# Kernel tuning notes

Hardware: AMD Instinct MI355X
Metric: run time of the kernel (lower is better)

## Reference

```python
import jax, jax.numpy as jnp
import numpy as np

EPS = 1e-12  # matches torch.nn.functional.normalize default eps

def _l2_normalize(x):
    # F.normalize: x / max(||x||_2, eps)
    n = jnp.linalg.norm(x, axis=-1, keepdims=True)
    return x / jnp.maximum(n, EPS)

def setup_inputs() -> dict:
    key = jax.random.key(0)
    k_z, k_e = jax.random.split(key)
    B, N, D, K = 8, 4096, 64, 8192
    z = jax.random.normal(k_z, (B, N, D), dtype=jnp.float32)
    # nn.Embedding weight initialized uniform(-1/K, 1/K)
    embedding = jax.random.uniform(k_e, (K, D), dtype=jnp.float32,
                                   minval=-1.0 / K, maxval=1.0 / K)
    return {"z": z, "embedding": embedding, "temperature": 1.0}

def reference(z, embedding, temperature):
    z_norm = _l2_normalize(z)                      # (B,N,D)
    codebook = _l2_normalize(embedding)            # (K,D)
    sim = jnp.einsum('bnd,kd->bnk', z_norm, codebook)  # (B,N,K)
    dists = 1.0 - sim
    probs = jax.nn.softmax(-dists / temperature, axis=-1)  # (B,N,K)
    z_q = jnp.einsum('bnk,kd->bnd', probs, codebook)       # (B,N,D)
    return (probs, z_q)
```

## Files before the change

### kernel.cpp

```cpp
#include <hip/hip_runtime.h>
#include <hip/hip_bf16.h>


#define M_TOTAL 32768
#define KCODES  8192
#define DDIM    64
#define KSPLIT  4
#define KCHUNK  (KCODES / KSPLIT)

typedef __attribute__((ext_vector_type(8))) short bf16x8;
typedef __attribute__((ext_vector_type(4))) float f32x4;

#define LDS_BARRIER() asm volatile("s_waitcnt lgkmcnt(0)\ns_barrier" ::: "memory")

__device__ inline unsigned short f2bf(float x) {
  union { float f; unsigned u; } v; v.f = x;
  unsigned r = v.u + 0x7FFFu + ((v.u >> 16) & 1u);
  return (unsigned short)(r >> 16);
}

__global__ __launch_bounds__(256) void norm_rows_kernel(
    const float* __restrict__ in, unsigned short* __restrict__ F,
    unsigned short* __restrict__ FT, int nrows) {
  int row = blockIdx.x * 4 + (threadIdx.x >> 6);
  int d = threadIdx.x & 63;
  if (row >= nrows) return;
  float x = in[(size_t)row * DDIM + d];
  float s = x * x;
  s += __shfl_xor(s, 1);  s += __shfl_xor(s, 2);  s += __shfl_xor(s, 4);
  s += __shfl_xor(s, 8);  s += __shfl_xor(s, 16); s += __shfl_xor(s, 32);
  float scale = 1.0f / fmaxf(sqrtf(s), 1e-12f);
  unsigned short b = f2bf(x * scale);
  {
    int blk = row >> 4, ml = row & 15;
    int h = d >> 5, g = (d >> 3) & 3, j = d & 7;
    F[((size_t)(blk * 2 + h)) * 512 + (g * 16 + ml) * 8 + j] = b;
  }
  if (FT) {
    int ds = d >> 4, dl = d & 15;
    int kb = row >> 5, kg = (row >> 3) & 3, kj = row & 7;
    FT[((size_t)(kb * 4 + ds)) * 512 + (kg * 16 + dl) * 8 + kj] = b;
  }
}

__global__ __launch_bounds__(512, 4) void pass1_kernel(
    const unsigned short* __restrict__ FZn,
    const unsigned short* __restrict__ FCb,
    const float* __restrict__ tptr,
    float* __restrict__ rsp) {
  __shared__ __align__(16) unsigned short sbuf[2][4096];
  const int tid = threadIdx.x;
  const int w  = tid >> 6, l = tid & 63, g = l >> 4, ml = l & 15;
  const int rb = blockIdx.x & 127;
  const int ks = blockIdx.x >> 7;
  const int mA = rb * 256 + w * 32;
  const int mB = mA + 16;
  const int k0 = ks * KCHUNK;
  const float sc = 1.4426950408889634f / tptr[0];

  const unsigned short* fz = FZn + ((size_t)((rb * 16 + w * 2) * 2)) * 512;
  const bf16x8 zA0 = *(const bf16x8*)(fz + l * 8);
  const bf16x8 zA1 = *(const bf16x8*)(fz + 512 + l * 8);
  const bf16x8 zB0 = *(const bf16x8*)(fz + 1024 + l * 8);
  const bf16x8 zB1 = *(const bf16x8*)(fz + 1536 + l * 8);

  const f32x4 zero = {0.f, 0.f, 0.f, 0.f};
  float rsA = 0.f, rsB = 0.f;

  const unsigned short* gb = FCb + (size_t)tid * 8;
  bf16x8 stg = *(const bf16x8*)(gb + (size_t)k0 * 64);
  int cur = 0;

  const int NIT = KCHUNK / 64;
  for (int it = 0; it < NIT; ++it) {
    *(bf16x8*)&sbuf[cur][tid * 8] = stg;
    if (it + 1 < NIT)
      stg = *(const bf16x8*)(gb + (size_t)(k0 + (it + 1) * 64) * 64);
    LDS_BARRIER();
    const unsigned short* sb = &sbuf[cur][0];
#pragma unroll
    for (int cb = 0; cb < 4; ++cb) {
      const bf16x8 c0 = *(const bf16x8*)(sb + cb * 1024 + l * 8);
      const bf16x8 c1 = *(const bf16x8*)(sb + cb * 1024 + 512 + l * 8);
      f32x4 aA = __builtin_amdgcn_mfma_f32_16x16x32_bf16(c0, zA0, zero, 0, 0, 0);
      aA = __builtin_amdgcn_mfma_f32_16x16x32_bf16(c1, zA1, aA, 0, 0, 0);
      f32x4 aB = __builtin_amdgcn_mfma_f32_16x16x32_bf16(c0, zB0, zero, 0, 0, 0);
      aB = __builtin_amdgcn_mfma_f32_16x16x32_bf16(c1, zB1, aB, 0, 0, 0);
      rsA += (exp2f((aA[0] - 1.0f) * sc) + exp2f((aA[1] - 1.0f) * sc))
           + (exp2f((aA[2] - 1.0f) * sc) + exp2f((aA[3] - 1.0f) * sc));
      rsB += (exp2f((aB[0] - 1.0f) * sc) + exp2f((aB[1] - 1.0f) * sc))
           + (exp2f((aB[2] - 1.0f) * sc) + exp2f((aB[3] - 1.0f) * sc));
    }
    cur ^= 1;
  }

  rsA += __shfl_xor(rsA, 16);  rsA += __shfl_xor(rsA, 32);
  rsB += __shfl_xor(rsB, 16);  rsB += __shfl_xor(rsB, 32);
  if (g == 0) {
    rsp[(size_t)ks * M_TOTAL + mA + ml] = rsA;
    rsp[(size_t)ks * M_TOTAL + mB + ml] = rsB;
  }
}

__global__ __launch_bounds__(256) void rs_kernel(
    const float* __restrict__ rsp, float* __restrict__ rs) {
  int m = blockIdx.x * 256 + threadIdx.x;
  float s = 0.f;
#pragma unroll
  for (int ks = 0; ks < KSPLIT; ++ks) s += rsp[(size_t)ks * M_TOTAL + m];
  rs[m] = s;
}

__global__ __launch_bounds__(512, 2) void pass2_kernel(
    const unsigned short* __restrict__ FZn,
    const unsigned short* __restrict__ FCb,
    const unsigned short* __restrict__ FCbT,
    const float* __restrict__ tptr,
    const float* __restrict__ rsv,
    float* __restrict__ probs,
    float* __restrict__ Up) {
  __shared__ __align__(16) unsigned short sbuf[2][4096];
  __shared__ __align__(16) unsigned short etile[8][16 * 56];
  const int tid = threadIdx.x;
  const int w  = tid >> 6, l = tid & 63, g = l >> 4, ml = l & 15;
  const int rb = blockIdx.x & 255;
  const int ks = blockIdx.x >> 8;
  const int m_base = rb * 128 + w * 16;
  const int k0 = ks * KCHUNK;
  const float sc = 1.4426950408889634f / tptr[0];

  const unsigned short* fz = FZn + ((size_t)((rb * 8 + w) * 2)) * 512;
  const bf16x8 zn0 = *(const bf16x8*)(fz + l * 8);
  const bf16x8 zn1 = *(const bf16x8*)(fz + 512 + l * 8);
  const float inv = 1.0f / rsv[m_base + ml];
  const f32x4 zero = {0.f, 0.f, 0.f, 0.f};
  f32x4 uacc[4] = {zero, zero, zero, zero};
  float* prow = probs + (size_t)(m_base + ml) * KCODES;

  const unsigned short* gb = (tid < 256 ? FCb : FCbT) + (size_t)(tid & 255) * 8;
  bf16x8 stg = *(const bf16x8*)(gb + (size_t)k0 * 64);
  int cur = 0;

  const int NIT = KCHUNK / 32;
  for (int it = 0; it < NIT; ++it) {
    *(bf16x8*)&sbuf[cur][tid * 8] = stg;
    if (it + 1 < NIT)
      stg = *(const bf16x8*)(gb + (size_t)(k0 + (it + 1) * 32) * 64);
    LDS_BARRIER();
    const unsigned short* sb = &sbuf[cur][0];
    const int kc = k0 + it * 32;
#pragma unroll
    for (int cs = 0; cs < 2; ++cs) {
      const bf16x8 c0 = *(const bf16x8*)(sb + cs * 1024 + l * 8);
      const bf16x8 c1 = *(const bf16x8*)(sb + cs * 1024 + 512 + l * 8);
      f32x4 a = __builtin_amdgcn_mfma_f32_16x16x32_bf16(c0, zn0, zero, 0, 0, 0);
      a = __builtin_amdgcn_mfma_f32_16x16x32_bf16(c1, zn1, a, 0, 0, 0);
      f32x4 p;
      p[0] = exp2f((a[0] - 1.0f) * sc) * inv;
      p[1] = exp2f((a[1] - 1.0f) * sc) * inv;
      p[2] = exp2f((a[2] - 1.0f) * sc) * inv;
      p[3] = exp2f((a[3] - 1.0f) * sc) * inv;
      *(f32x4*)(prow + kc + cs * 16 + g * 4) = p;
      union { __hip_bfloat162 hh[2]; uint2 u; } pk;
      pk.hh[0] = __float22bfloat162_rn(make_float2(p[0], p[1]));
      pk.hh[1] = __float22bfloat162_rn(make_float2(p[2], p[3]));
      *(uint2*)&etile[w][ml * 56 + cs * 16 + g * 4] = pk.u;
    }
    asm volatile("s_waitcnt lgkmcnt(0)" ::: "memory");
    const bf16x8 ef = *(const bf16x8*)&etile[w][ml * 56 + g * 8];
#pragma unroll
    for (int ds = 0; ds < 4; ++ds) {
      const bf16x8 ct = *(const bf16x8*)(sb + 2048 + ds * 512 + l * 8);
      uacc[ds] = __builtin_amdgcn_mfma_f32_16x16x32_bf16(ct, ef, uacc[ds], 0, 0, 0);
    }
    cur ^= 1;
  }

  float* urow = Up + ((size_t)ks * M_TOTAL + m_base + ml) * DDIM;
#pragma unroll
  for (int ds = 0; ds < 4; ++ds)
    *(f32x4*)(urow + ds * 16 + g * 4) = uacc[ds];
}

__global__ __launch_bounds__(256) void zq_kernel(
    const float* __restrict__ Up, float* __restrict__ zq) {
  size_t i = (size_t)blockIdx.x * 256 + threadIdx.x;
  f32x4 u = *(const f32x4*)(Up + i * 4);
#pragma unroll
  for (int ks = 1; ks < KSPLIT; ++ks) {
    f32x4 p = *(const f32x4*)(Up + (size_t)ks * M_TOTAL * DDIM + i * 4);
#pragma unroll
    for (int r = 0; r < 4; ++r) u[r] += p[r];
  }
  *(f32x4*)(zq + i * 4) = u;
}

extern "C" void kernel_launch(void* const* d_in, const int* in_sizes, int n_in,
                              void* d_out, int out_size, void* d_ws, size_t ws_size,
                              hipStream_t stream) {
  const float* z    = (const float*)d_in[0];
  const float* emb  = (const float*)d_in[1];
  const float* temp = (const float*)d_in[2];

  float* probs = (float*)d_out;
  float* zq    = probs + (size_t)M_TOTAL * KCODES;

  unsigned short* FZn  = (unsigned short*)d_ws;
  unsigned short* FCb  = FZn + (size_t)M_TOTAL * DDIM;
  unsigned short* FCbT = FCb + (size_t)KCODES * DDIM;
  float* Up  = (float*)(FCbT + (size_t)KCODES * DDIM);
  float* rsp = Up + (size_t)KSPLIT * M_TOTAL * DDIM;
  float* rs  = rsp + (size_t)KSPLIT * M_TOTAL;

  norm_rows_kernel<<<M_TOTAL / 4, 256, 0, stream>>>(z, FZn, nullptr, M_TOTAL);
  norm_rows_kernel<<<KCODES / 4, 256, 0, stream>>>(emb, FCb, FCbT, KCODES);
  pass1_kernel<<<128 * KSPLIT, 512, 0, stream>>>(FZn, FCb, temp, rsp);
  rs_kernel<<<M_TOTAL / 256, 256, 0, stream>>>(rsp, rs);
  pass2_kernel<<<256 * KSPLIT, 512, 0, stream>>>(FZn, FCb, FCbT, temp, rs, probs, Up);
  zq_kernel<<<(M_TOTAL * DDIM / 4) / 256, 256, 0, stream>>>(Up, zq);
}
```

Baseline: 369.6 us.

## Software-pipeline pass2 zq MFMA over triple-buffered LDS and fold scaling into FMA bias

In pass2, the probs-times-codebook MFMA for the previous tile is deferred to the next iteration, after the barrier. It reads from a third LDS buffer so the etile write and read are separated by a barrier and the lgkmcnt wait inside the loop goes away. The exp argument is also folded into a single FMA with a per-row log2 bias, which replaces the separate multiply by the inverse row sum; pass1 gets the same FMA treatment. The launch bounds are raised to 8 waves per SIMD hint, which may constrain registers and cause spills, and LDS use grows by one buffer.

```diff
diff --git a/kernel.cpp b/kernel.cpp
--- a/kernel.cpp
+++ b/kernel.cpp
@@ -57,6 +57,7 @@
   const int mB = mA + 16;
   const int k0 = ks * KCHUNK;
   const float sc = 1.4426950408889634f / tptr[0];
+  const float nb = -sc;
 
   const unsigned short* fz = FZn + ((size_t)((rb * 16 + w * 2) * 2)) * 512;
   const bf16x8 zA0 = *(const bf16x8*)(fz + l * 8);
@@ -86,10 +87,10 @@
       aA = __builtin_amdgcn_mfma_f32_16x16x32_bf16(c1, zA1, aA, 0, 0, 0);
       f32x4 aB = __builtin_amdgcn_mfma_f32_16x16x32_bf16(c0, zB0, zero, 0, 0, 0);
       aB = __builtin_amdgcn_mfma_f32_16x16x32_bf16(c1, zB1, aB, 0, 0, 0);
-      rsA += (exp2f((aA[0] - 1.0f) * sc) + exp2f((aA[1] - 1.0f) * sc))
-           + (exp2f((aA[2] - 1.0f) * sc) + exp2f((aA[3] - 1.0f) * sc));
-      rsB += (exp2f((aB[0] - 1.0f) * sc) + exp2f((aB[1] - 1.0f) * sc))
-           + (exp2f((aB[2] - 1.0f) * sc) + exp2f((aB[3] - 1.0f) * sc));
+      rsA += (exp2f(fmaf(aA[0], sc, nb)) + exp2f(fmaf(aA[1], sc, nb)))
+           + (exp2f(fmaf(aA[2], sc, nb)) + exp2f(fmaf(aA[3], sc, nb)));
+      rsB += (exp2f(fmaf(aB[0], sc, nb)) + exp2f(fmaf(aB[1], sc, nb)))
+           + (exp2f(fmaf(aB[2], sc, nb)) + exp2f(fmaf(aB[3], sc, nb)));
     }
     cur ^= 1;
   }
@@ -111,7 +112,7 @@
   rs[m] = s;
 }
 
-__global__ __launch_bounds__(512, 2) void pass2_kernel(
+__global__ __launch_bounds__(512, 8) void pass2_kernel(
     const unsigned short* __restrict__ FZn,
     const unsigned short* __restrict__ FCb,
     const unsigned short* __restrict__ FCbT,
@@ -119,7 +120,7 @@
     const float* __restrict__ rsv,
     float* __restrict__ probs,
     float* __restrict__ Up) {
-  __shared__ __align__(16) unsigned short sbuf[2][4096];
+  __shared__ __align__(16) unsigned short sbuf[3][4096];
   __shared__ __align__(16) unsigned short etile[8][16 * 56];
   const int tid = threadIdx.x;
   const int w  = tid >> 6, l = tid & 63, g = l >> 4, ml = l & 15;
@@ -132,21 +133,30 @@
   const unsigned short* fz = FZn + ((size_t)((rb * 8 + w) * 2)) * 512;
   const bf16x8 zn0 = *(const bf16x8*)(fz + l * 8);
   const bf16x8 zn1 = *(const bf16x8*)(fz + 512 + l * 8);
-  const float inv = 1.0f / rsv[m_base + ml];
+  const float bias = -sc - log2f(rsv[m_base + ml]);
   const f32x4 zero = {0.f, 0.f, 0.f, 0.f};
   f32x4 uacc[4] = {zero, zero, zero, zero};
   float* prow = probs + (size_t)(m_base + ml) * KCODES;
 
   const unsigned short* gb = (tid < 256 ? FCb : FCbT) + (size_t)(tid & 255) * 8;
   bf16x8 stg = *(const bf16x8*)(gb + (size_t)k0 * 64);
-  int cur = 0;
 
   const int NIT = KCHUNK / 32;
+  int cur = 0, prev = 2;
   for (int it = 0; it < NIT; ++it) {
     *(bf16x8*)&sbuf[cur][tid * 8] = stg;
     if (it + 1 < NIT)
       stg = *(const bf16x8*)(gb + (size_t)(k0 + (it + 1) * 32) * 64);
     LDS_BARRIER();
+    if (it) {
+      const unsigned short* sbp = &sbuf[prev][0];
+      const bf16x8 ef = *(const bf16x8*)&etile[w][ml * 56 + g * 8];
+#pragma unroll
+      for (int ds = 0; ds < 4; ++ds) {
+        const bf16x8 ct = *(const bf16x8*)(sbp + 2048 + ds * 512 + l * 8);
+        uacc[ds] = __builtin_amdgcn_mfma_f32_16x16x32_bf16(ct, ef, uacc[ds], 0, 0, 0);
+      }
+    }
     const unsigned short* sb = &sbuf[cur][0];
     const int kc = k0 + it * 32;
 #pragma unroll
@@ -156,24 +166,28 @@
       f32x4 a = __builtin_amdgcn_mfma_f32_16x16x32_bf16(c0, zn0, zero, 0, 0, 0);
       a = __builtin_amdgcn_mfma_f32_16x16x32_bf16(c1, zn1, a, 0, 0, 0);
       f32x4 p;
-      p[0] = exp2f((a[0] - 1.0f) * sc) * inv;
-      p[1] = exp2f((a[1] - 1.0f) * sc) * inv;
-      p[2] = exp2f((a[2] - 1.0f) * sc) * inv;
-      p[3] = exp2f((a[3] - 1.0f) * sc) * inv;
+      p[0] = exp2f(fmaf(a[0], sc, bias));
+      p[1] = exp2f(fmaf(a[1], sc, bias));
+      p[2] = exp2f(fmaf(a[2], sc, bias));
+      p[3] = exp2f(fmaf(a[3], sc, bias));
       *(f32x4*)(prow + kc + cs * 16 + g * 4) = p;
       union { __hip_bfloat162 hh[2]; uint2 u; } pk;
       pk.hh[0] = __float22bfloat162_rn(make_float2(p[0], p[1]));
       pk.hh[1] = __float22bfloat162_rn(make_float2(p[2], p[3]));
       *(uint2*)&etile[w][ml * 56 + cs * 16 + g * 4] = pk.u;
     }
+    prev = cur;
+    cur = (cur == 2) ? 0 : cur + 1;
+  }
+  {
+    const unsigned short* sbp = &sbuf[prev][0];
     asm volatile("s_waitcnt lgkmcnt(0)" ::: "memory");
     const bf16x8 ef = *(const bf16x8*)&etile[w][ml * 56 + g * 8];
 #pragma unroll
     for (int ds = 0; ds < 4; ++ds) {
-      const bf16x8 ct = *(const bf16x8*)(sb + 2048 + ds * 512 + l * 8);
+      const bf16x8 ct = *(const bf16x8*)(sbp + 2048 + ds * 512 + l * 8);
       uacc[ds] = __builtin_amdgcn_mfma_f32_16x16x32_bf16(ct, ef, uacc[ds], 0, 0, 0);
     }
-    cur ^= 1;
   }
 
   float* urow = Up + ((size_t)ks * M_TOTAL + m_base + ml) * DDIM;
```

After: 505.2 us. +36.7%, slower.
